# Performance work log

Measured on AMD Instinct MI355X. Metric: run time of the kernel, lower is better.

Reference implementation:

```python
import jax, jax.numpy as jnp
import numpy as np

B, S, D_IN, D_OUT = 512, 512, 256, 256  # batch, seq(=n_unit), in_dim, out_dim

def setup_inputs() -> dict:
    key = jax.random.key(0)
    k1, k2, k3 = jax.random.split(key, 3)
    scale = 1.0 / np.sqrt(D_IN)
    x = jax.random.normal(k1, (B, S, D_IN), dtype=jnp.float32)
    Wx = jax.random.normal(k2, (S, D_IN, D_OUT), dtype=jnp.float32) * scale
    Wh = jax.random.normal(k3, (S, D_OUT, D_OUT), dtype=jnp.float32) * scale
    return {"x": x, "Wx": Wx, "Wh": Wh}

def reference(x, Wx, Wh):
    # Per-timestep unique RNN cell: h_t = tanh(x_t @ Wx[t] + h_{t-1} @ Wh[t]);
    # h_{-1} = 0 (original passes h=None at idx==0, i.e. zero hidden).
    def step(h, inp):
        xt, wx, wh = inp  # xt: [B, D_IN], wx: [D_IN, D_OUT], wh: [D_OUT, D_OUT]
        h_new = jnp.tanh(xt @ wx + h @ wh)
        return h_new, h_new
    x_t = jnp.transpose(x, (1, 0, 2))  # [S, B, D_IN]
    h0 = jnp.zeros((x.shape[0], Wh.shape[-1]), dtype=x.dtype)
    _, outs = jax.lax.scan(step, h0, (x_t, Wx, Wh))  # outs: [S, B, D_OUT]
    return jnp.transpose(outs, (1, 0, 2))  # [B, S, D_OUT]
```

## Files before the change

### kernel.cpp

```cpp
#include <hip/hip_runtime.h>
#include <math.h>

#define S_LEN 512
#define B_SZ  512
#define D_DIM 256

__device__ __forceinline__ float tanh_fast(float x) {
    float e = __expf(2.0f * x);
    return 1.0f - 2.0f / (e + 1.0f);
}

__global__ __launch_bounds__(256, 2) void phase1_xwx(const float* __restrict__ x,
                                                     const float* __restrict__ Wx,
                                                     float* __restrict__ Z) {
    const int t   = blockIdx.x;
    const int b0  = blockIdx.y * 16;
    const int tid = threadIdx.x;
    const int c4  = (tid & 63) * 4;
    const int ks  = tid >> 6;
    const int kbase = ks * 64;

    __shared__ float xs[16][D_DIM];
    __shared__ float red[4][16][D_DIM];

    #pragma unroll
    for (int r4 = 0; r4 < 4; ++r4) {
        int idx = r4 * 256 + tid;
        int r   = idx >> 6;
        int cc  = (idx & 63) * 4;
        *(float4*)&xs[r][cc] =
            *(const float4*)(x + ((size_t)(b0 + r) * S_LEN + t) * D_DIM + cc);
    }
    __syncthreads();

    float4 acc[16];
    #pragma unroll
    for (int r = 0; r < 16; ++r) acc[r] = make_float4(0.f, 0.f, 0.f, 0.f);

    const float* wp = Wx + (size_t)t * D_DIM * D_DIM + c4;

    #pragma unroll 2
    for (int k4 = 0; k4 < 16; ++k4) {
        const int k = kbase + k4 * 4;
        const float4 w0 = *(const float4*)(wp + (size_t)(k + 0) * D_DIM);
        const float4 w1 = *(const float4*)(wp + (size_t)(k + 1) * D_DIM);
        const float4 w2 = *(const float4*)(wp + (size_t)(k + 2) * D_DIM);
        const float4 w3 = *(const float4*)(wp + (size_t)(k + 3) * D_DIM);
        #pragma unroll
        for (int r = 0; r < 16; ++r) {
            const float4 xv = *(const float4*)&xs[r][k];
            acc[r].x = fmaf(xv.x, w0.x, acc[r].x);
            acc[r].y = fmaf(xv.x, w0.y, acc[r].y);
            acc[r].z = fmaf(xv.x, w0.z, acc[r].z);
            acc[r].w = fmaf(xv.x, w0.w, acc[r].w);
            acc[r].x = fmaf(xv.y, w1.x, acc[r].x);
            acc[r].y = fmaf(xv.y, w1.y, acc[r].y);
            acc[r].z = fmaf(xv.y, w1.z, acc[r].z);
            acc[r].w = fmaf(xv.y, w1.w, acc[r].w);
            acc[r].x = fmaf(xv.z, w2.x, acc[r].x);
            acc[r].y = fmaf(xv.z, w2.y, acc[r].y);
            acc[r].z = fmaf(xv.z, w2.z, acc[r].z);
            acc[r].w = fmaf(xv.z, w2.w, acc[r].w);
            acc[r].x = fmaf(xv.w, w3.x, acc[r].x);
            acc[r].y = fmaf(xv.w, w3.y, acc[r].y);
            acc[r].z = fmaf(xv.w, w3.z, acc[r].z);
            acc[r].w = fmaf(xv.w, w3.w, acc[r].w);
        }
    }

    #pragma unroll
    for (int r = 0; r < 16; ++r)
        *(float4*)&red[ks][r][c4] = acc[r];
    __syncthreads();

    #pragma unroll
    for (int i = 0; i < 4; ++i) {
        const int r = ks + i * 4;
        const float4 s0 = *(const float4*)&red[0][r][c4];
        const float4 s1 = *(const float4*)&red[1][r][c4];
        const float4 s2 = *(const float4*)&red[2][r][c4];
        const float4 s3 = *(const float4*)&red[3][r][c4];
        float4 s;
        s.x = ((s0.x + s1.x) + s2.x) + s3.x;
        s.y = ((s0.y + s1.y) + s2.y) + s3.y;
        s.z = ((s0.z + s1.z) + s2.z) + s3.z;
        s.w = ((s0.w + s1.w) + s2.w) + s3.w;
        *(float4*)(Z + ((size_t)(b0 + r) * S_LEN + t) * D_DIM + c4) = s;
    }
}

__global__ __launch_bounds__(1024) void phase2_scan(const float* __restrict__ Wh,
                                                    float* __restrict__ ZH) {
    const int g   = blockIdx.x;
    const int b0  = g * 2;
    const int tid = threadIdx.x;
    const int c4  = (tid & 63) * 4;
    const int ks  = tid >> 6;
    const int kbase = ks * 16;
    const int rm  = (tid >> 8) & 1;
    const int rc  = tid & 255;

    __shared__ float h[2][D_DIM];
    __shared__ float red[16][2][D_DIM];

    for (int i = tid; i < 2 * D_DIM; i += 1024) ((float*)h)[i] = 0.0f;
    __syncthreads();

    float* zrow = ZH + ((size_t)(b0 + rm) * S_LEN) * D_DIM + rc;
    const float* wb = Wh + c4;

    for (int t = 0; t < S_LEN; ++t) {
        float z = 0.0f;
        if (tid < 512) z = zrow[(size_t)t * D_DIM];

        const float* wt = wb + (size_t)t * D_DIM * D_DIM;
        float4 w[16];
        #pragma unroll
        for (int i = 0; i < 16; ++i)
            w[i] = *(const float4*)(wt + (size_t)(kbase + i) * D_DIM);

        float4 acc0 = make_float4(0.f, 0.f, 0.f, 0.f);
        float4 acc1 = make_float4(0.f, 0.f, 0.f, 0.f);
        #pragma unroll
        for (int q = 0; q < 4; ++q) {
            const float4 ha = *(const float4*)&h[0][kbase + q * 4];
            const float4 hb = *(const float4*)&h[1][kbase + q * 4];
            const float4 w0 = w[q * 4 + 0];
            const float4 w1 = w[q * 4 + 1];
            const float4 w2 = w[q * 4 + 2];
            const float4 w3 = w[q * 4 + 3];
            acc0.x = fmaf(ha.x, w0.x, acc0.x);
            acc0.y = fmaf(ha.x, w0.y, acc0.y);
            acc0.z = fmaf(ha.x, w0.z, acc0.z);
            acc0.w = fmaf(ha.x, w0.w, acc0.w);
            acc0.x = fmaf(ha.y, w1.x, acc0.x);
            acc0.y = fmaf(ha.y, w1.y, acc0.y);
            acc0.z = fmaf(ha.y, w1.z, acc0.z);
            acc0.w = fmaf(ha.y, w1.w, acc0.w);
            acc0.x = fmaf(ha.z, w2.x, acc0.x);
            acc0.y = fmaf(ha.z, w2.y, acc0.y);
            acc0.z = fmaf(ha.z, w2.z, acc0.z);
            acc0.w = fmaf(ha.z, w2.w, acc0.w);
            acc0.x = fmaf(ha.w, w3.x, acc0.x);
            acc0.y = fmaf(ha.w, w3.y, acc0.y);
            acc0.z = fmaf(ha.w, w3.z, acc0.z);
            acc0.w = fmaf(ha.w, w3.w, acc0.w);

            acc1.x = fmaf(hb.x, w0.x, acc1.x);
            acc1.y = fmaf(hb.x, w0.y, acc1.y);
            acc1.z = fmaf(hb.x, w0.z, acc1.z);
            acc1.w = fmaf(hb.x, w0.w, acc1.w);
            acc1.x = fmaf(hb.y, w1.x, acc1.x);
            acc1.y = fmaf(hb.y, w1.y, acc1.y);
            acc1.z = fmaf(hb.y, w1.z, acc1.z);
            acc1.w = fmaf(hb.y, w1.w, acc1.w);
            acc1.x = fmaf(hb.z, w2.x, acc1.x);
            acc1.y = fmaf(hb.z, w2.y, acc1.y);
            acc1.z = fmaf(hb.z, w2.z, acc1.z);
            acc1.w = fmaf(hb.z, w2.w, acc1.w);
            acc1.x = fmaf(hb.w, w3.x, acc1.x);
            acc1.y = fmaf(hb.w, w3.y, acc1.y);
            acc1.z = fmaf(hb.w, w3.z, acc1.z);
            acc1.w = fmaf(hb.w, w3.w, acc1.w);
        }

        *(float4*)&red[ks][0][c4] = acc0;
        *(float4*)&red[ks][1][c4] = acc1;
        __syncthreads();

        if (tid < 512) {
            float s = z;
            #pragma unroll
            for (int sl = 0; sl < 16; ++sl) s += red[sl][rm][rc];
            const float hv = tanh_fast(s);
            h[rm][rc] = hv;
            zrow[(size_t)t * D_DIM] = hv;
        }
        __syncthreads();
    }
}

extern "C" void kernel_launch(void* const* d_in, const int* in_sizes, int n_in,
                              void* d_out, int out_size, void* d_ws, size_t ws_size,
                              hipStream_t stream) {
    const float* x  = (const float*)d_in[0];
    const float* Wx = (const float*)d_in[1];
    const float* Wh = (const float*)d_in[2];
    float* out = (float*)d_out;

    phase1_xwx<<<dim3(S_LEN, B_SZ / 16), 256, 0, stream>>>(x, Wx, out);
    phase2_scan<<<dim3(B_SZ / 2), 1024, 0, stream>>>(Wh, out);
}
```

Baseline: 3.125 ms.

## Double batch rows per block in both phases to increase weight reuse

```diff
diff --git a/kernel.cpp b/kernel.cpp
--- a/kernel.cpp
+++ b/kernel.cpp
@@ -14,18 +14,18 @@
                                                      const float* __restrict__ Wx,
                                                      float* __restrict__ Z) {
     const int t   = blockIdx.x;
-    const int b0  = blockIdx.y * 16;
+    const int b0  = blockIdx.y * 32;
     const int tid = threadIdx.x;
     const int c4  = (tid & 63) * 4;
     const int ks  = tid >> 6;
     const int kbase = ks * 64;
 
-    __shared__ float xs[16][D_DIM];
-    __shared__ float red[4][16][D_DIM];
+    __shared__ float xs[32][D_DIM];
+    __shared__ float red[4][8][D_DIM];
 
     #pragma unroll
-    for (int r4 = 0; r4 < 4; ++r4) {
-        int idx = r4 * 256 + tid;
+    for (int i = 0; i < 8; ++i) {
+        int idx = i * 256 + tid;
         int r   = idx >> 6;
         int cc  = (idx & 63) * 4;
         *(float4*)&xs[r][cc] =
@@ -33,9 +33,9 @@
     }
     __syncthreads();
 
-    float4 acc[16];
+    float4 acc[32];
     #pragma unroll
-    for (int r = 0; r < 16; ++r) acc[r] = make_float4(0.f, 0.f, 0.f, 0.f);
+    for (int r = 0; r < 32; ++r) acc[r] = make_float4(0.f, 0.f, 0.f, 0.f);
 
     const float* wp = Wx + (size_t)t * D_DIM * D_DIM + c4;
 
@@ -47,7 +47,7 @@
         const float4 w2 = *(const float4*)(wp + (size_t)(k + 2) * D_DIM);
         const float4 w3 = *(const float4*)(wp + (size_t)(k + 3) * D_DIM);
         #pragma unroll
-        for (int r = 0; r < 16; ++r) {
+        for (int r = 0; r < 32; ++r) {
             const float4 xv = *(const float4*)&xs[r][k];
             acc[r].x = fmaf(xv.x, w0.x, acc[r].x);
             acc[r].y = fmaf(xv.x, w0.y, acc[r].y);
@@ -69,49 +69,52 @@
     }
 
     #pragma unroll
-    for (int r = 0; r < 16; ++r)
-        *(float4*)&red[ks][r][c4] = acc[r];
-    __syncthreads();
-
-    #pragma unroll
-    for (int i = 0; i < 4; ++i) {
-        const int r = ks + i * 4;
-        const float4 s0 = *(const float4*)&red[0][r][c4];
-        const float4 s1 = *(const float4*)&red[1][r][c4];
-        const float4 s2 = *(const float4*)&red[2][r][c4];
-        const float4 s3 = *(const float4*)&red[3][r][c4];
-        float4 s;
-        s.x = ((s0.x + s1.x) + s2.x) + s3.x;
-        s.y = ((s0.y + s1.y) + s2.y) + s3.y;
-        s.z = ((s0.z + s1.z) + s2.z) + s3.z;
-        s.w = ((s0.w + s1.w) + s2.w) + s3.w;
-        *(float4*)(Z + ((size_t)(b0 + r) * S_LEN + t) * D_DIM + c4) = s;
+    for (int ch = 0; ch < 4; ++ch) {
+        #pragma unroll
+        for (int rl = 0; rl < 8; ++rl)
+            *(float4*)&red[ks][rl][c4] = acc[ch * 8 + rl];
+        __syncthreads();
+        #pragma unroll
+        for (int i = 0; i < 2; ++i) {
+            const int rl = ks * 2 + i;
+            const int r  = ch * 8 + rl;
+            const float4 s0 = *(const float4*)&red[0][rl][c4];
+            const float4 s1 = *(const float4*)&red[1][rl][c4];
+            const float4 s2 = *(const float4*)&red[2][rl][c4];
+            const float4 s3 = *(const float4*)&red[3][rl][c4];
+            float4 s;
+            s.x = ((s0.x + s1.x) + s2.x) + s3.x;
+            s.y = ((s0.y + s1.y) + s2.y) + s3.y;
+            s.z = ((s0.z + s1.z) + s2.z) + s3.z;
+            s.w = ((s0.w + s1.w) + s2.w) + s3.w;
+            *(float4*)(Z + ((size_t)(b0 + r) * S_LEN + t) * D_DIM + c4) = s;
+        }
+        __syncthreads();
     }
 }
 
-__global__ __launch_bounds__(1024) void phase2_scan(const float* __restrict__ Wh,
-                                                    float* __restrict__ ZH) {
+__global__ __launch_bounds__(1024, 4) void phase2_scan(const float* __restrict__ Wh,
+                                                       float* __restrict__ ZH) {
     const int g   = blockIdx.x;
-    const int b0  = g * 2;
+    const int b0  = g * 4;
     const int tid = threadIdx.x;
     const int c4  = (tid & 63) * 4;
     const int ks  = tid >> 6;
     const int kbase = ks * 16;
-    const int rm  = (tid >> 8) & 1;
+    const int rm  = tid >> 8;
     const int rc  = tid & 255;
 
-    __shared__ float h[2][D_DIM];
-    __shared__ float red[16][2][D_DIM];
+    __shared__ float h[4][D_DIM];
+    __shared__ float red[16][4][D_DIM];
 
-    for (int i = tid; i < 2 * D_DIM; i += 1024) ((float*)h)[i] = 0.0f;
+    for (int i = tid; i < 4 * D_DIM; i += 1024) ((float*)h)[i] = 0.0f;
     __syncthreads();
 
     float* zrow = ZH + ((size_t)(b0 + rm) * S_LEN) * D_DIM + rc;
     const float* wb = Wh + c4;
 
     for (int t = 0; t < S_LEN; ++t) {
-        float z = 0.0f;
-        if (tid < 512) z = zrow[(size_t)t * D_DIM];
+        const float z = zrow[(size_t)t * D_DIM];
 
         const float* wt = wb + (size_t)t * D_DIM * D_DIM;
         float4 w[16];
@@ -119,63 +122,43 @@
         for (int i = 0; i < 16; ++i)
             w[i] = *(const float4*)(wt + (size_t)(kbase + i) * D_DIM);
 
-        float4 acc0 = make_float4(0.f, 0.f, 0.f, 0.f);
-        float4 acc1 = make_float4(0.f, 0.f, 0.f, 0.f);
+        float4 acc[4];
+        #pragma unroll
+        for (int m = 0; m < 4; ++m) acc[m] = make_float4(0.f, 0.f, 0.f, 0.f);
+
         #pragma unroll
         for (int q = 0; q < 4; ++q) {
-            const float4 ha = *(const float4*)&h[0][kbase + q * 4];
-            const float4 hb = *(const float4*)&h[1][kbase + q * 4];
-            const float4 w0 = w[q * 4 + 0];
-            const float4 w1 = w[q * 4 + 1];
-            const float4 w2 = w[q * 4 + 2];
-            const float4 w3 = w[q * 4 + 3];
-            acc0.x = fmaf(ha.x, w0.x, acc0.x);
-            acc0.y = fmaf(ha.x, w0.y, acc0.y);
-            acc0.z = fmaf(ha.x, w0.z, acc0.z);
-            acc0.w = fmaf(ha.x, w0.w, acc0.w);
-            acc0.x = fmaf(ha.y, w1.x, acc0.x);
-            acc0.y = fmaf(ha.y, w1.y, acc0.y);
-            acc0.z = fmaf(ha.y, w1.z, acc0.z);
-            acc0.w = fmaf(ha.y, w1.w, acc0.w);
-            acc0.x = fmaf(ha.z, w2.x, acc0.x);
-            acc0.y = fmaf(ha.z, w2.y, acc0.y);
-            acc0.z = fmaf(ha.z, w2.z, acc0.z);
-            acc0.w = fmaf(ha.z, w2.w, acc0.w);
-            acc0.x = fmaf(ha.w, w3.x, acc0.x);
-            acc0.y = fmaf(ha.w, w3.y, acc0.y);
-            acc0.z = fmaf(ha.w, w3.z, acc0.z);
-            acc0.w = fmaf(ha.w, w3.w, acc0.w);
-
-            acc1.x = fmaf(hb.x, w0.x, acc1.x);
-            acc1.y = fmaf(hb.x, w0.y, acc1.y);
-            acc1.z = fmaf(hb.x, w0.z, acc1.z);
-            acc1.w = fmaf(hb.x, w0.w, acc1.w);
-            acc1.x = fmaf(hb.y, w1.x, acc1.x);
-            acc1.y = fmaf(hb.y, w1.y, acc1.y);
-            acc1.z = fmaf(hb.y, w1.z, acc1.z);
-            acc1.w = fmaf(hb.y, w1.w, acc1.w);
-            acc1.x = fmaf(hb.z, w2.x, acc1.x);
-            acc1.y = fmaf(hb.z, w2.y, acc1.y);
-            acc1.z = fmaf(hb.z, w2.z, acc1.z);
-            acc1.w = fmaf(hb.z, w2.w, acc1.w);
-            acc1.x = fmaf(hb.w, w3.x, acc1.x);
-            acc1.y = fmaf(hb.w, w3.y, acc1.y);
-            acc1.z = fmaf(hb.w, w3.z, acc1.z);
-            acc1.w = fmaf(hb.w, w3.w, acc1.w);
+            float4 hq[4];
+            #pragma unroll
+            for (int m = 0; m < 4; ++m)
+                hq[m] = *(const float4*)&h[m][kbase + q * 4];
+            #pragma unroll
+            for (int j = 0; j < 4; ++j) {
+                const float4 wj = w[q * 4 + j];
+                #pragma unroll
+                for (int m = 0; m < 4; ++m) {
+                    const float hv = (j == 0) ? hq[m].x :
+                                     (j == 1) ? hq[m].y :
+                                     (j == 2) ? hq[m].z : hq[m].w;
+                    acc[m].x = fmaf(hv, wj.x, acc[m].x);
+                    acc[m].y = fmaf(hv, wj.y, acc[m].y);
+                    acc[m].z = fmaf(hv, wj.z, acc[m].z);
+                    acc[m].w = fmaf(hv, wj.w, acc[m].w);
+                }
+            }
         }
 
-        *(float4*)&red[ks][0][c4] = acc0;
-        *(float4*)&red[ks][1][c4] = acc1;
+        #pragma unroll
+        for (int m = 0; m < 4; ++m)
+            *(float4*)&red[ks][m][c4] = acc[m];
         __syncthreads();
 
-        if (tid < 512) {
-            float s = z;
-            #pragma unroll
-            for (int sl = 0; sl < 16; ++sl) s += red[sl][rm][rc];
-            const float hv = tanh_fast(s);
-            h[rm][rc] = hv;
-            zrow[(size_t)t * D_DIM] = hv;
-        }
+        float s = z;
+        #pragma unroll
+        for (int sl = 0; sl < 16; ++sl) s += red[sl][rm][rc];
+        const float hv = tanh_fast(s);
+        h[rm][rc] = hv;
+        zrow[(size_t)t * D_DIM] = hv;
         __syncthreads();
     }
 }
@@ -188,6 +171,6 @@
     const float* Wh = (const float*)d_in[2];
     float* out = (float*)d_out;
 
-    phase1_xwx<<<dim3(S_LEN, B_SZ / 16), 256, 0, stream>>>(x, Wx, out);
-    phase2_scan<<<dim3(B_SZ / 2), 1024, 0, stream>>>(Wh, out);
+    phase1_xwx<<<dim3(S_LEN, B_SZ / 32), 256, 0, stream>>>(x, Wx, out);
+    phase2_scan<<<dim3(B_SZ / 4), 1024, 0, stream>>>(Wh, out);
 }
```

Result: slower. 7.745 ms (+147.9%).

## Halve scan block size with deeper per-thread K slices and deferred stores

Applied to the files above, without the earlier changes.

```diff
diff --git a/kernel.cpp b/kernel.cpp
--- a/kernel.cpp
+++ b/kernel.cpp
@@ -89,95 +89,76 @@
     }
 }
 
-__global__ __launch_bounds__(1024) void phase2_scan(const float* __restrict__ Wh,
-                                                    float* __restrict__ ZH) {
+__global__ __launch_bounds__(512, 2) void phase2_scan(const float* __restrict__ Wh,
+                                                      float* __restrict__ ZH) {
     const int g   = blockIdx.x;
     const int b0  = g * 2;
     const int tid = threadIdx.x;
     const int c4  = (tid & 63) * 4;
     const int ks  = tid >> 6;
-    const int kbase = ks * 16;
-    const int rm  = (tid >> 8) & 1;
+    const int kbase = ks * 32;
+    const int rm  = tid >> 8;
     const int rc  = tid & 255;
 
     __shared__ float h[2][D_DIM];
-    __shared__ float red[16][2][D_DIM];
+    __shared__ float red[8][2][D_DIM];
 
-    for (int i = tid; i < 2 * D_DIM; i += 1024) ((float*)h)[i] = 0.0f;
+    for (int i = tid; i < 2 * D_DIM; i += 512) ((float*)h)[i] = 0.0f;
     __syncthreads();
 
     float* zrow = ZH + ((size_t)(b0 + rm) * S_LEN) * D_DIM + rc;
     const float* wb = Wh + c4;
 
+    float hv_prev = 0.0f;
+
     for (int t = 0; t < S_LEN; ++t) {
-        float z = 0.0f;
-        if (tid < 512) z = zrow[(size_t)t * D_DIM];
+        if (t > 0) zrow[(size_t)(t - 1) * D_DIM] = hv_prev;
+
+        const float z = zrow[(size_t)t * D_DIM];
 
         const float* wt = wb + (size_t)t * D_DIM * D_DIM;
-        float4 w[16];
+        float4 w[32];
         #pragma unroll
-        for (int i = 0; i < 16; ++i)
+        for (int i = 0; i < 32; ++i)
             w[i] = *(const float4*)(wt + (size_t)(kbase + i) * D_DIM);
 
         float4 acc0 = make_float4(0.f, 0.f, 0.f, 0.f);
         float4 acc1 = make_float4(0.f, 0.f, 0.f, 0.f);
         #pragma unroll
-        for (int q = 0; q < 4; ++q) {
+        for (int q = 0; q < 8; ++q) {
             const float4 ha = *(const float4*)&h[0][kbase + q * 4];
             const float4 hb = *(const float4*)&h[1][kbase + q * 4];
-            const float4 w0 = w[q * 4 + 0];
-            const float4 w1 = w[q * 4 + 1];
-            const float4 w2 = w[q * 4 + 2];
-            const float4 w3 = w[q * 4 + 3];
-            acc0.x = fmaf(ha.x, w0.x, acc0.x);
-            acc0.y = fmaf(ha.x, w0.y, acc0.y);
-            acc0.z = fmaf(ha.x, w0.z, acc0.z);
-            acc0.w = fmaf(ha.x, w0.w, acc0.w);
-            acc0.x = fmaf(ha.y, w1.x, acc0.x);
-            acc0.y = fmaf(ha.y, w1.y, acc0.y);
-            acc0.z = fmaf(ha.y, w1.z, acc0.z);
-            acc0.w = fmaf(ha.y, w1.w, acc0.w);
-            acc0.x = fmaf(ha.z, w2.x, acc0.x);
-            acc0.y = fmaf(ha.z, w2.y, acc0.y);
-            acc0.z = fmaf(ha.z, w2.z, acc0.z);
-            acc0.w = fmaf(ha.z, w2.w, acc0.w);
-            acc0.x = fmaf(ha.w, w3.x, acc0.x);
-            acc0.y = fmaf(ha.w, w3.y, acc0.y);
-            acc0.z = fmaf(ha.w, w3.z, acc0.z);
-            acc0.w = fmaf(ha.w, w3.w, acc0.w);
-
-            acc1.x = fmaf(hb.x, w0.x, acc1.x);
-            acc1.y = fmaf(hb.x, w0.y, acc1.y);
-            acc1.z = fmaf(hb.x, w0.z, acc1.z);
-            acc1.w = fmaf(hb.x, w0.w, acc1.w);
-            acc1.x = fmaf(hb.y, w1.x, acc1.x);
-            acc1.y = fmaf(hb.y, w1.y, acc1.y);
-            acc1.z = fmaf(hb.y, w1.z, acc1.z);
-            acc1.w = fmaf(hb.y, w1.w, acc1.w);
-            acc1.x = fmaf(hb.z, w2.x, acc1.x);
-            acc1.y = fmaf(hb.z, w2.y, acc1.y);
-            acc1.z = fmaf(hb.z, w2.z, acc1.z);
-            acc1.w = fmaf(hb.z, w2.w, acc1.w);
-            acc1.x = fmaf(hb.w, w3.x, acc1.x);
-            acc1.y = fmaf(hb.w, w3.y, acc1.y);
-            acc1.z = fmaf(hb.w, w3.z, acc1.z);
-            acc1.w = fmaf(hb.w, w3.w, acc1.w);
+            #pragma unroll
+            for (int j = 0; j < 4; ++j) {
+                const float4 wj = w[q * 4 + j];
+                const float hva = (j == 0) ? ha.x : (j == 1) ? ha.y :
+                                  (j == 2) ? ha.z : ha.w;
+                const float hvb = (j == 0) ? hb.x : (j == 1) ? hb.y :
+                                  (j == 2) ? hb.z : hb.w;
+                acc0.x = fmaf(hva, wj.x, acc0.x);
+                acc0.y = fmaf(hva, wj.y, acc0.y);
+                acc0.z = fmaf(hva, wj.z, acc0.z);
+                acc0.w = fmaf(hva, wj.w, acc0.w);
+                acc1.x = fmaf(hvb, wj.x, acc1.x);
+                acc1.y = fmaf(hvb, wj.y, acc1.y);
+                acc1.z = fmaf(hvb, wj.z, acc1.z);
+                acc1.w = fmaf(hvb, wj.w, acc1.w);
+            }
         }
 
         *(float4*)&red[ks][0][c4] = acc0;
         *(float4*)&red[ks][1][c4] = acc1;
         __syncthreads();
 
-        if (tid < 512) {
-            float s = z;
-            #pragma unroll
-            for (int sl = 0; sl < 16; ++sl) s += red[sl][rm][rc];
-            const float hv = tanh_fast(s);
-            h[rm][rc] = hv;
-            zrow[(size_t)t * D_DIM] = hv;
-        }
+        float s = z;
+        #pragma unroll
+        for (int sl = 0; sl < 8; ++sl) s += red[sl][rm][rc];
+        const float hv = tanh_fast(s);
+        h[rm][rc] = hv;
+        hv_prev = hv;
         __syncthreads();
     }
+    zrow[(size_t)(S_LEN - 1) * D_DIM] = hv_prev;
 }
 
 extern "C" void kernel_launch(void* const* d_in, const int* in_sizes, int n_in,
@@ -189,5 +170,5 @@
     float* out = (float*)d_out;
 
     phase1_xwx<<<dim3(S_LEN, B_SZ / 16), 256, 0, stream>>>(x, Wx, out);
-    phase2_scan<<<dim3(B_SZ / 2), 1024, 0, stream>>>(Wh, out);
+    phase2_scan<<<dim3(B_SZ / 2), 512, 0, stream>>>(Wh, out);
 }
```

After: 3.972 ms. 1.27x slower.
